# Kernel tuning notes

Measured on AMD Instinct MI355X. Metric: run time of the kernel, lower is better.

## Reference

```python
import jax, jax.numpy as jnp
import numpy as np
import math

T, B = 2048, 32
N_CLASSES = 64
D_MODEL = 512
N_LAYERS = 2
N_HEADS = 8
D_HEAD = 64
D_FF = N_HEADS * D_HEAD * 4  # 2048
E_VAL = (D_MODEL + 1) // 2   # 256 value-embedding dim
D_PE = D_MODEL // 2          # 256 positional dim (concatenated)
EPS_ATTN = 1e-6
EPS_LN = 1e-5


def _pe_table(t, d):
    pos = np.arange(t, dtype=np.float32)[:, None]
    div = np.exp(np.arange(0, d, 2, dtype=np.float32) * (-math.log(10000.0) / d))
    pe = np.zeros((t, d), dtype=np.float32)
    pe[:, 0::2] = np.sin(pos * div)
    pe[:, 1::2] = np.cos(pos * div)
    return jnp.asarray(pe)


def _ln(h, g, b):
    m = jnp.mean(h, axis=-1, keepdims=True)
    v = jnp.mean((h - m) ** 2, axis=-1, keepdims=True)
    return (h - m) * jax.lax.rsqrt(v + EPS_LN) * g + b


def setup_inputs() -> dict:
    key = jax.random.key(0)
    ks = jax.random.split(key, 12)
    s = 0.02
    L, dm, dff = N_LAYERS, D_MODEL, D_FF
    return {
        "x": jax.random.randint(ks[0], (T, B), 0, N_CLASSES),
        "E": jax.random.normal(ks[1], (N_CLASSES, E_VAL)) * s,
        "Wq": jax.random.normal(ks[2], (L, dm, dm)) * s, "bq": jnp.zeros((L, dm)),
        "Wk": jax.random.normal(ks[3], (L, dm, dm)) * s, "bk": jnp.zeros((L, dm)),
        "Wv": jax.random.normal(ks[4], (L, dm, dm)) * s, "bv": jnp.zeros((L, dm)),
        "Wo": jax.random.normal(ks[5], (L, dm, dm)) * s, "bo": jnp.zeros((L, dm)),
        "g1": jnp.ones((L, dm)), "be1": jnp.zeros((L, dm)),
        "W1": jax.random.normal(ks[6], (L, dm, dff)) * s, "b1": jnp.zeros((L, dff)),
        "W2": jax.random.normal(ks[7], (L, dff, dm)) * s, "b2": jnp.zeros((L, dm)),
        "g2": jnp.ones((L, dm)), "be2": jnp.zeros((L, dm)),
        "Wp": jax.random.normal(ks[8], (dm, N_CLASSES)) * s, "bp": jnp.zeros((N_CLASSES,)),
    }


def reference(x, E, Wq, bq, Wk, bk, Wv, bv, Wo, bo, g1, be1, W1, b1, W2, b2, g2, be2, Wp, bp):
    # embed tokens: x [T,B] -> [T,B,E_VAL]; concat positional (broadcast over batch) -> [T,B,D_MODEL]
    emb = E[x]
    pe = _pe_table(T, D_PE)
    h0 = jnp.concatenate([emb, jnp.broadcast_to(pe[:, None, :], (T, B, D_PE))], axis=-1)

    Si0 = jnp.zeros((N_LAYERS, B, N_HEADS, D_HEAD, D_HEAD), h0.dtype)  # sum_t k \otimes v
    Zi0 = jnp.zeros((N_LAYERS, B, N_HEADS, D_HEAD), h0.dtype)          # sum_t k

    phi = lambda u: jax.nn.elu(u) + 1.0  # linear-attention feature map

    def step(carry, xt):
        Si, Zi = carry
        h = xt  # [B, D_MODEL]
        for l in range(N_LAYERS):
            q = phi((h @ Wq[l] + bq[l]).reshape(B, N_HEADS, D_HEAD))
            k = phi((h @ Wk[l] + bk[l]).reshape(B, N_HEADS, D_HEAD))
            v = (h @ Wv[l] + bv[l]).reshape(B, N_HEADS, D_HEAD)
            Sl = Si[l] + k[..., :, None] * v[..., None, :]   # [B,H,D,D]
            Zl = Zi[l] + k
            num = jnp.einsum("bhd,bhdm->bhm", q, Sl)
            den = jnp.einsum("bhd,bhd->bh", q, Zl) + EPS_ATTN
            attn = (num / den[..., None]).reshape(B, N_HEADS * D_HEAD) @ Wo[l] + bo[l]
            h = _ln(h + attn, g1[l], be1[l])
            ff = jax.nn.relu(h @ W1[l] + b1[l]) @ W2[l] + b2[l]
            h = _ln(h + ff, g2[l], be2[l])
            Si = Si.at[l].set(Sl)
            Zi = Zi.at[l].set(Zl)
        return (Si, Zi), h

    _, ys = jax.lax.scan(step, (Si0, Zi0), h0)       # [T,B,D_MODEL]
    y_hat = jnp.transpose(ys, (1, 0, 2)) @ Wp + bp   # [B,T,N_CLASSES]
    return y_hat
```

## Files before the change

### kernel.cpp

```cpp
#include <hip/hip_runtime.h>


typedef unsigned short u16;
typedef __bf16 bf16x8 __attribute__((ext_vector_type(8)));
typedef float f32x4 __attribute__((ext_vector_type(4)));
typedef float f32x16 __attribute__((ext_vector_type(16)));

#define T_SEQ 2048
#define BATCH 32
#define NHEADS 8
#define CT 64
#define NCHUNK 32

#define SKEW(r, k) ((((k) + (((r) >> 3) << 3))) & 63)

__device__ __forceinline__ float b2f(u16 u) {
    union { unsigned int i; float f; } v; v.i = ((unsigned int)u) << 16; return v.f;
}
__device__ __forceinline__ u16 f2b(float f) {
    union { __bf16 b; u16 u; } v; v.b = (__bf16)f; return v.u;
}

__device__ __forceinline__ void gl_lds16(const u16* g, u16* l) {
    __builtin_amdgcn_global_load_lds(
        (const __attribute__((address_space(1))) void*)g,
        (__attribute__((address_space(3))) void*)l,
        16, 0, 0);
}

template<int ACT, bool RES>
__global__ __launch_bounds__(512, 2) void gemm_p8(
    const u16* __restrict__ A, const u16* __restrict__ BT,
    const float* __restrict__ bias, const u16* __restrict__ R,
    u16* __restrict__ C,
    int M, int N, int K, int act_split, int nbn, int GM)
{
    __shared__ __align__(16) u16 AsS[2][256 * 64];
    __shared__ __align__(16) u16 BsS[2][256 * 64];

    const int bid = blockIdx.x;
    const int gsz = GM * nbn;
    const int grp = bid / gsz, rm = bid % gsz;
    const int bm = (grp * GM + rm % GM) * 256;
    const int bn = (rm / GM) * 256;
    if (bm >= M || bn >= N) return;

    const int tid = threadIdx.x;
    const int lane = tid & 63;
    const int w  = tid >> 6;
    const int wr = w >> 2;
    const int wc = w & 3;
    const int l32 = lane & 31;
    const int kh  = lane >> 5;
    const int sr = lane >> 3;
    const int sg = lane & 7;

    const int NT = K >> 6;

    f32x16 acc[4][2] = {};

    auto stage64 = [&](u16* lds, const u16* g, int rowbase, int k0, int row0) {
        const int r = row0 + w * 8 + sr;
        const int gs = sg ^ (r & 7);
        gl_lds16(g + (size_t)(rowbase + r) * K + k0 + gs * 8,
                 lds + (row0 + w * 8) * 64);
    };

    #pragma unroll
    for (int qq = 0; qq < 4; qq++) stage64(AsS[0], A, bm, 0, qq * 64);
    #pragma unroll
    for (int qq = 0; qq < 4; qq++) stage64(BsS[0], BT, bn, 0, qq * 64);
    #pragma unroll
    for (int qq = 0; qq < 4; qq++) stage64(AsS[1], A, bm, 64, qq * 64);
    #pragma unroll
    for (int qq = 0; qq < 4; qq++) stage64(BsS[1], BT, bn, 64, qq * 64);
    asm volatile("s_waitcnt vmcnt(8)" ::: "memory");
    __builtin_amdgcn_s_barrier();

    bf16x8 af[2][4], b0[4], b1[4];

    for (int t = 0; t < NT; ++t) {
        u16* As_ = AsS[t & 1];
        u16* Bs_ = BsS[t & 1];
        const int k2 = (t + 2) << 6;
        const bool pf = (t + 2) < NT;

        #pragma unroll
        for (int mf = 0; mf < 2; mf++) {
            const int r = wr * 128 + mf * 32 + l32;
            #pragma unroll
            for (int ks = 0; ks < 4; ks++) {
                const int gq = (ks * 2 + kh) ^ (r & 7);
                af[mf][ks] = *(const bf16x8*)&As_[r * 64 + gq * 8];
            }
        }
        {
            const int rb = wc * 64 + l32;
            #pragma unroll
            for (int ks = 0; ks < 4; ks++) {
                const int gq = (ks * 2 + kh) ^ (rb & 7);
                b0[ks] = *(const bf16x8*)&Bs_[rb * 64 + gq * 8];
            }
        }
        __builtin_amdgcn_s_barrier();
        asm volatile("s_waitcnt lgkmcnt(0)" ::: "memory");
        __builtin_amdgcn_sched_barrier(0);
        __builtin_amdgcn_s_setprio(1);
        #pragma unroll
        for (int ks = 0; ks < 4; ks++)
            #pragma unroll
            for (int mf = 0; mf < 2; mf++)
                acc[mf][0] = __builtin_amdgcn_mfma_f32_32x32x16_bf16(
                    af[mf][ks], b0[ks], acc[mf][0], 0, 0, 0);
        __builtin_amdgcn_s_setprio(0);
        __builtin_amdgcn_s_barrier();

        {
            const int rb = wc * 64 + 32 + l32;
            #pragma unroll
            for (int ks = 0; ks < 4; ks++) {
                const int gq = (ks * 2 + kh) ^ (rb & 7);
                b1[ks] = *(const bf16x8*)&Bs_[rb * 64 + gq * 8];
            }
        }
        if (pf) { stage64(As_, A, bm, k2, 0); stage64(As_, A, bm, k2, 128); }
        __builtin_amdgcn_s_barrier();
        asm volatile("s_waitcnt lgkmcnt(0)" ::: "memory");
        __builtin_amdgcn_sched_barrier(0);
        __builtin_amdgcn_s_setprio(1);
        #pragma unroll
        for (int ks = 0; ks < 4; ks++)
            #pragma unroll
            for (int mf = 0; mf < 2; mf++)
                acc[mf][1] = __builtin_amdgcn_mfma_f32_32x32x16_bf16(
                    af[mf][ks], b1[ks], acc[mf][1], 0, 0, 0);
        __builtin_amdgcn_s_setprio(0);
        __builtin_amdgcn_s_barrier();

        #pragma unroll
        for (int mf = 0; mf < 2; mf++) {
            const int r = wr * 128 + 64 + mf * 32 + l32;
            #pragma unroll
            for (int ks = 0; ks < 4; ks++) {
                const int gq = (ks * 2 + kh) ^ (r & 7);
                af[mf][ks] = *(const bf16x8*)&As_[r * 64 + gq * 8];
            }
        }
        if (pf) { stage64(Bs_, BT, bn, k2, 0); stage64(Bs_, BT, bn, k2, 64); }
        __builtin_amdgcn_s_barrier();
        asm volatile("s_waitcnt lgkmcnt(0)" ::: "memory");
        __builtin_amdgcn_sched_barrier(0);
        __builtin_amdgcn_s_setprio(1);
        #pragma unroll
        for (int ks = 0; ks < 4; ks++)
            #pragma unroll
            for (int mf = 0; mf < 2; mf++)
                acc[2 + mf][0] = __builtin_amdgcn_mfma_f32_32x32x16_bf16(
                    af[mf][ks], b0[ks], acc[2 + mf][0], 0, 0, 0);
        __builtin_amdgcn_s_setprio(0);
        __builtin_amdgcn_s_barrier();

        if (pf) {
            stage64(Bs_, BT, bn, k2, 128); stage64(Bs_, BT, bn, k2, 192);
            stage64(As_, A,  bm, k2, 64);  stage64(As_, A,  bm, k2, 192);
        }
        __builtin_amdgcn_s_barrier();
        __builtin_amdgcn_s_setprio(1);
        #pragma unroll
        for (int ks = 0; ks < 4; ks++)
            #pragma unroll
            for (int mf = 0; mf < 2; mf++)
                acc[2 + mf][1] = __builtin_amdgcn_mfma_f32_32x32x16_bf16(
                    af[mf][ks], b1[ks], acc[2 + mf][1], 0, 0, 0);
        __builtin_amdgcn_s_setprio(0);
        if (pf) asm volatile("s_waitcnt vmcnt(8)" ::: "memory");
        else    asm volatile("s_waitcnt vmcnt(0)" ::: "memory");
        __builtin_amdgcn_s_barrier();
    }

    #pragma unroll
    for (int i = 0; i < 4; i++) {
        const int row0 = bm + wr * 128 + i * 32 + 4 * kh;
        #pragma unroll
        for (int j = 0; j < 2; j++) {
            const int col = bn + wc * 64 + j * 32 + l32;
            const float bb = bias[col];
            const bool phi = (ACT == 2) && (col < act_split);
            #pragma unroll
            for (int reg = 0; reg < 16; reg++) {
                const int m = row0 + (reg & 3) + 8 * (reg >> 2);
                float v = acc[i][j][reg] + bb;
                if (RES) v += b2f(R[(size_t)m * N + col]);
                if (ACT == 1) v = fmaxf(v, 0.f);
                if (ACT == 2) { if (phi) v = (v > 0.f) ? (v + 1.f) : __expf(v); }
                C[(size_t)m * N + col] = f2b(v);
            }
        }
    }
}

template<int BM, int BN, int WM, int WN>
__global__ __launch_bounds__(WM*WN*64) void gemm_sm(
    const u16* __restrict__ A, const u16* __restrict__ BT,
    const float* __restrict__ bias, float* __restrict__ C,
    int M, int N, int K)
{
    constexpr int BK = 32;
    constexpr int LDT = BK + 8;
    constexpr int NTHR = WM * WN * 64;
    __shared__ __align__(16) u16 As[BM * LDT];
    __shared__ __align__(16) u16 Bs[BN * LDT];

    const int tid = threadIdx.x;
    const int bm = blockIdx.y * BM;
    const int bn = blockIdx.x * BN;
    const int lane = tid & 63;
    const int wid = tid >> 6;
    const int wrow = (wid / WN) * (BM / WM);
    const int wcol = (wid % WN) * (BN / WN);
    constexpr int FM = BM / WM / 16;
    constexpr int FN = BN / WN / 16;
    const int lrow = lane & 15;
    const int lk = (lane >> 4) * 8;

    f32x4 acc[FM][FN] = {};

    for (int k0 = 0; k0 < K; k0 += BK) {
        #pragma unroll
        for (int g0 = 0; g0 < BM * 4; g0 += NTHR) {
            int g = g0 + tid;
            int row = g >> 2, kk = (g & 3) * 8;
            *(uint4*)&As[row * LDT + kk] =
                *(const uint4*)&A[(size_t)(bm + row) * K + k0 + kk];
        }
        #pragma unroll
        for (int g0 = 0; g0 < BN * 4; g0 += NTHR) {
            int g = g0 + tid;
            int row = g >> 2, kk = (g & 3) * 8;
            *(uint4*)&Bs[row * LDT + kk] =
                *(const uint4*)&BT[(size_t)(bn + row) * K + k0 + kk];
        }
        __syncthreads();
        bf16x8 af[FM], bfv[FN];
        #pragma unroll
        for (int i = 0; i < FM; i++)
            af[i] = *(const bf16x8*)&As[(wrow + i * 16 + lrow) * LDT + lk];
        #pragma unroll
        for (int j = 0; j < FN; j++)
            bfv[j] = *(const bf16x8*)&Bs[(wcol + j * 16 + lrow) * LDT + lk];
        #pragma unroll
        for (int i = 0; i < FM; i++)
            #pragma unroll
            for (int j = 0; j < FN; j++)
                acc[i][j] = __builtin_amdgcn_mfma_f32_16x16x32_bf16(
                    bfv[j], af[i], acc[i][j], 0, 0, 0);
        __syncthreads();
    }

    #pragma unroll
    for (int i = 0; i < FM; i++) {
        const int row = bm + wrow + i * 16 + lrow;
        #pragma unroll
        for (int j = 0; j < FN; j++) {
            const int col0 = bn + wcol + j * 16 + (lane >> 4) * 4;
            const float4 bb = *(const float4*)&bias[col0];
            float4 o = { acc[i][j][0] + bb.x, acc[i][j][1] + bb.y,
                         acc[i][j][2] + bb.z, acc[i][j][3] + bb.w };
            *(float4*)&C[(size_t)row * N + col0] = o;
        }
    }
}

__global__ __launch_bounds__(256) void prep_kernel(
    const float* __restrict__ Wq, const float* __restrict__ Wk,
    const float* __restrict__ Wv, const float* __restrict__ Wo,
    const float* __restrict__ W1, const float* __restrict__ W2,
    const float* __restrict__ Wp,
    const float* __restrict__ bq, const float* __restrict__ bk,
    const float* __restrict__ bv,
    u16* __restrict__ qkvT, u16* __restrict__ woT, u16* __restrict__ w1T,
    u16* __restrict__ w2T, u16* __restrict__ wpT, u16* __restrict__ pe,
    float* __restrict__ bqkv)
{
    __shared__ float tile[32][33];
    const int bid = blockIdx.x;
    const float* src; u16* dst; int K, N, bx, by;

    if (bid < 1536) {
        int l = bid / 768, r = bid % 768, m = r >> 8, t = r & 255;
        const float* s3[3] = { Wq, Wk, Wv };
        src = s3[m] + (size_t)l * 262144;
        dst = qkvT + (size_t)l * 786432 + (size_t)m * 262144;
        K = 512; N = 512; bx = t & 15; by = t >> 4;
    } else if (bid < 2048) {
        int r = bid - 1536, l = r >> 8, t = r & 255;
        src = Wo + (size_t)l * 262144; dst = woT + (size_t)l * 262144;
        K = 512; N = 512; bx = t & 15; by = t >> 4;
    } else if (bid < 4096) {
        int r = bid - 2048, l = r >> 10, t = r & 1023;
        src = W1 + (size_t)l * 1048576; dst = w1T + (size_t)l * 1048576;
        K = 512; N = 2048; bx = t & 63; by = t >> 6;
    } else if (bid < 6144) {
        int r = bid - 4096, l = r >> 10, t = r & 1023;
        src = W2 + (size_t)l * 1048576; dst = w2T + (size_t)l * 1048576;
        K = 2048; N = 512; bx = t & 15; by = t >> 4;
    } else if (bid < 6176) {
        int t = bid - 6144;
        src = Wp; dst = wpT; K = 512; N = 64; bx = t & 1; by = t >> 1;
    } else if (bid < 8224) {
        int id = (bid - 6176) * 256 + threadIdx.x;
        int t = id >> 8, j = id & 255;
        int i = j >> 1;
        float div = expf(-(float)(2 * i) * (9.210340371976184f / 256.f));
        float arg = (float)t * div;
        pe[id] = f2b((j & 1) ? cosf(arg) : sinf(arg));
        return;
    } else {
        int id = (bid - 8224) * 256 + threadIdx.x;
        if (id < 3072) {
            int l = id / 1536, i2 = id % 1536;
            float v = (i2 < 512) ? bq[l * 512 + i2]
                    : (i2 < 1024) ? bk[l * 512 + i2 - 512]
                                  : bv[l * 512 + i2 - 1024];
            bqkv[id] = v;
        }
        return;
    }

    int tx = threadIdx.x & 31, ty = threadIdx.x >> 5;
    #pragma unroll
    for (int yy = 0; yy < 4; yy++) {
        int k = by * 32 + ty + yy * 8;
        tile[ty + yy * 8][tx] = src[(size_t)k * N + bx * 32 + tx];
    }
    __syncthreads();
    #pragma unroll
    for (int yy = 0; yy < 4; yy++) {
        int n = bx * 32 + ty + yy * 8;
        dst[(size_t)n * K + by * 32 + tx] = f2b(tile[tx][ty + yy * 8]);
    }
}

__global__ __launch_bounds__(256) void embed_kernel(
    const int* __restrict__ x, const float* __restrict__ E,
    const u16* __restrict__ pe, u16* __restrict__ h, int b0)
{
    int idx = blockIdx.x * 256 + threadIdx.x;
    int e8 = idx * 8;
    int r = e8 >> 9;
    int c = e8 & 511;
    int t = r & (T_SEQ - 1);
    int b = b0 + (r >> 11);
    union { u16 u[8]; uint4 v; } o;
    if (c < 256) {
        const float* Ep = &E[(size_t)x[t * BATCH + b] * 256 + c];
        #pragma unroll
        for (int i = 0; i < 8; i++) o.u[i] = f2b(Ep[i]);
    } else {
        o.v = *(const uint4*)&pe[t * 256 + (c - 256)];
    }
    *(uint4*)&h[e8] = o.v;
}

__global__ __launch_bounds__(256) void attn_chunk_sums(
    const u16* __restrict__ qkv, u16* __restrict__ S, float* __restrict__ Z,
    int BHg)
{
    __shared__ __align__(16) u16 Kt[64 * 72], Vt[64 * 72];
    int bid = blockIdx.x;
    int bh = bid % BHg, c = bid / BHg;
    int bl = bh >> 3, hh = bh & 7;
    {
        const int m  = threadIdx.x & 7;
        const int d0 = m * 8;
        #pragma unroll
        for (int p = 0; p < 2; p++) {
            const int t = p * 32 + (threadIdx.x >> 3);
            size_t rr = ((size_t)(bl * T_SEQ + c * 64 + t)) * 1536 + hh * 64 + d0;
            uint4 kv = *(const uint4*)&qkv[rr + 512];
            uint4 vv = *(const uint4*)&qkv[rr + 1024];
            const u16* kp = (const u16*)&kv;
            const u16* vp = (const u16*)&vv;
            const int sk = (t + d0) & 63;
            u16* kb = &Kt[d0 * 72 + sk];
            u16* vb = &Vt[d0 * 72 + sk];
            #pragma unroll
            for (int s = 0; s < 8; s++) { kb[s * 72] = kp[s]; vb[s * 72] = vp[s]; }
        }
    }
    __syncthreads();
    int lane = threadIdx.x & 63;
    int w = threadIdx.x >> 6;
    int lrow = lane & 15, quad = lane >> 4;
    int m0 = w * 16;
    f32x4 acc[4] = {};
    #pragma unroll
    for (int k0 = 0; k0 < 64; k0 += 32) {
        const int ra = m0 + lrow;
        bf16x8 af = *(const bf16x8*)&Vt[ra * 72 + SKEW(ra, k0 + quad * 8)];
        #pragma unroll
        for (int jt = 0; jt < 4; jt++) {
            const int rb = jt * 16 + lrow;
            bf16x8 bf = *(const bf16x8*)&Kt[rb * 72 + SKEW(rb, k0 + quad * 8)];
            acc[jt] = __builtin_amdgcn_mfma_f32_16x16x32_bf16(bf, af, acc[jt], 0, 0, 0);
        }
    }
    size_t base = ((size_t)c * BHg + bh) * 4096;
    const int m = m0 + lrow;
    #pragma unroll
    for (int jt = 0; jt < 4; jt++) {
        const int d0 = jt * 16 + quad * 4;
        union { u16 q[4]; uint2 u; } pk;
        #pragma unroll
        for (int r = 0; r < 4; r++) pk.q[r] = f2b(acc[jt][r]);
        *(uint2*)&S[base + m * 64 + d0] = pk.u;
    }
    if (threadIdx.x < 64) {
        const int d = threadIdx.x;
        float z = 0.f;
        #pragma unroll
        for (int t8 = 0; t8 < 64; t8 += 8) {
            bf16x8 kk = *(const bf16x8*)&Kt[d * 72 + SKEW(d, t8)];
            #pragma unroll
            for (int u = 0; u < 8; u++) z += (float)kk[u];
        }
        Z[((size_t)c * BHg + bh) * 64 + d] = z;
    }
}

__global__ __launch_bounds__(256) void attn_prefix(
    u16* __restrict__ S, float* __restrict__ Z, int BHg)
{
    int gid = blockIdx.x * 256 + threadIdx.x;
    int bh = gid >> 12, e = gid & 4095;
    size_t stride = (size_t)BHg * 4096;
    size_t base = (size_t)bh * 4096 + e;
    float v[NCHUNK];
    #pragma unroll
    for (int c = 0; c < NCHUNK; c++) v[c] = b2f(S[base + c * stride]);
    float run = 0.f;
    #pragma unroll
    for (int c = 0; c < NCHUNK; c++) {
        float t = v[c]; S[base + c * stride] = f2b(run); run += t;
    }
    if (gid < BHg * 64) {
        size_t zb = (size_t)gid;
        size_t zs = (size_t)BHg * 64;
        float zv[NCHUNK];
        #pragma unroll
        for (int c = 0; c < NCHUNK; c++) zv[c] = Z[zb + c * zs];
        float zr = 0.f;
        #pragma unroll
        for (int c = 0; c < NCHUNK; c++) {
            float t = zv[c]; Z[zb + c * zs] = zr; zr += t;
        }
    }
}

__global__ __launch_bounds__(256) void attn_intra(
    const u16* __restrict__ qkv, const u16* __restrict__ Sp,
    const float* __restrict__ Zp, u16* __restrict__ out, int BHg)
{
    __shared__ __align__(16) u16 Qs[64 * 72], Ks[64 * 72], Vt[64 * 72],
                                 Ssh[64 * 72];
    __shared__ float Zsh[64], den2sh[64], den1sh[64];
    u16* Ps = Ks;
    int bid = blockIdx.x;
    int bh = bid % BHg, c = bid / BHg;
    int bl = bh >> 3, hh = bh & 7;
    size_t sbase = ((size_t)c * BHg + bh) * 4096;
    {
        const int m  = threadIdx.x & 7;
        const int d0 = m * 8;
        #pragma unroll
        for (int p = 0; p < 2; p++) {
            const int t = p * 32 + (threadIdx.x >> 3);
            size_t rr = ((size_t)(bl * T_SEQ + c * 64 + t)) * 1536 + hh * 64 + d0;
            *(uint4*)&Qs[t * 72 + d0]  = *(const uint4*)&qkv[rr];
            *(uint4*)&Ks[t * 72 + d0]  = *(const uint4*)&qkv[rr + 512];
            *(uint4*)&Ssh[t * 72 + d0] = *(const uint4*)&Sp[sbase + t * 64 + d0];
            uint4 vv = *(const uint4*)&qkv[rr + 1024];
            const u16* vp = (const u16*)&vv;
            const int sk = (t + d0) & 63;
            u16* vb = &Vt[d0 * 72 + sk];
            #pragma unroll
            for (int s = 0; s < 8; s++) vb[s * 72] = vp[s];
        }
    }
    if (threadIdx.x < 64)
        Zsh[threadIdx.x] = Zp[((size_t)c * BHg + bh) * 64 + threadIdx.x];
    __syncthreads();

    if (threadIdx.x < 64) {
        float s = 0.f;
        #pragma unroll
        for (int d8 = 0; d8 < 64; d8 += 8) {
            bf16x8 qq = *(const bf16x8*)&Qs[threadIdx.x * 72 + d8];
            #pragma unroll
            for (int u = 0; u < 8; u++) s += (float)qq[u] * Zsh[d8 + u];
        }
        den2sh[threadIdx.x] = s;
    }

    int lane = threadIdx.x & 63;
    int w = threadIdx.x >> 6;
    int lrow = lane & 15, quad = lane >> 4;
    int i0 = w * 16;

    f32x4 accp[4] = {};
    #pragma unroll
    for (int k0 = 0; k0 < 64; k0 += 32) {
        bf16x8 af = *(const bf16x8*)&Qs[(i0 + lrow) * 72 + k0 + quad * 8];
        #pragma unroll
        for (int jt = 0; jt < 4; jt++) {
            bf16x8 bf = *(const bf16x8*)&Ks[(jt * 16 + lrow) * 72 + k0 + quad * 8];
            accp[jt] = __builtin_amdgcn_mfma_f32_16x16x32_bf16(af, bf, accp[jt], 0, 0, 0);
        }
    }
    __syncthreads();
    #pragma unroll
    for (int r = 0; r < 4; r++) {
        int row = i0 + quad * 4 + r;
        float d1 = 0.f;
        #pragma unroll
        for (int jt = 0; jt < 4; jt++) {
            int col = jt * 16 + lrow;
            float pv = (col <= row) ? accp[jt][r] : 0.f;
            d1 += pv;
            Ps[row * 72 + col] = f2b(pv);
        }
        #pragma unroll
        for (int off = 1; off < 16; off <<= 1)
            d1 += __shfl_xor(d1, off, 64);
        if (lrow == 0) den1sh[row] = d1;
    }
    __syncthreads();

    f32x4 acco[4] = {};
    #pragma unroll
    for (int k0 = 0; k0 < 64; k0 += 32) {
        bf16x8 ps = *(const bf16x8*)&Ps[(i0 + lrow) * 72 + k0 + quad * 8];
        #pragma unroll
        for (int jt = 0; jt < 4; jt++) {
            const int rv = jt * 16 + lrow;
            bf16x8 vf = *(const bf16x8*)&Vt[rv * 72 + SKEW(rv, k0 + quad * 8)];
            acco[jt] = __builtin_amdgcn_mfma_f32_16x16x32_bf16(vf, ps, acco[jt], 0, 0, 0);
        }
    }
    #pragma unroll
    for (int k0 = 0; k0 < 64; k0 += 32) {
        bf16x8 qf = *(const bf16x8*)&Qs[(i0 + lrow) * 72 + k0 + quad * 8];
        #pragma unroll
        for (int jt = 0; jt < 4; jt++) {
            bf16x8 sf = *(const bf16x8*)&Ssh[(jt * 16 + lrow) * 72 + k0 + quad * 8];
            acco[jt] = __builtin_amdgcn_mfma_f32_16x16x32_bf16(sf, qf, acco[jt], 0, 0, 0);
        }
    }
    const int i = i0 + lrow;
    const float inv = 1.f / (den1sh[i] + den2sh[i] + 1e-6f);
    size_t orow = ((size_t)(bl * T_SEQ + c * 64 + i)) * 512 + hh * 64;
    #pragma unroll
    for (int jt = 0; jt < 4; jt++) {
        const int m0 = jt * 16 + quad * 4;
        union { u16 q[4]; uint2 u; } pk;
        #pragma unroll
        for (int r = 0; r < 4; r++) pk.q[r] = f2b(acco[jt][r] * inv);
        *(uint2*)&out[orow + m0] = pk.u;
    }
}

__global__ __launch_bounds__(256) void ln_kernel(
    const u16* __restrict__ s_in,
    const float* __restrict__ g, const float* __restrict__ be, u16* __restrict__ out)
{
    int row = blockIdx.x * 4 + (threadIdx.x >> 6);
    int lane = threadIdx.x & 63;
    size_t base = (size_t)row * 512 + lane * 8;
    uint4 hv = *(const uint4*)&s_in[base];
    const u16* hp = (const u16*)&hv;
    float x[8]; float s = 0.f;
    #pragma unroll
    for (int i = 0; i < 8; i++) { x[i] = b2f(hp[i]); s += x[i]; }
    #pragma unroll
    for (int off = 32; off > 0; off >>= 1) s += __shfl_xor(s, off, 64);
    float m = s * (1.f / 512.f);
    float vs = 0.f;
    #pragma unroll
    for (int i = 0; i < 8; i++) { float t = x[i] - m; vs += t * t; }
    #pragma unroll
    for (int off = 32; off > 0; off >>= 1) vs += __shfl_xor(vs, off, 64);
    float rstd = rsqrtf(vs * (1.f / 512.f) + 1e-5f);
    union { u16 u[8]; uint4 v; } o;
    #pragma unroll
    for (int i = 0; i < 8; i++)
        o.u[i] = f2b((x[i] - m) * rstd * g[lane * 8 + i] + be[lane * 8 + i]);
    *(uint4*)&out[base] = o.v;
}

extern "C" void kernel_launch(void* const* d_in, const int* in_sizes, int n_in,
                              void* d_out, int out_size, void* d_ws, size_t ws_size,
                              hipStream_t stream)
{
    const int*   x  = (const int*)d_in[0];
    const float* E  = (const float*)d_in[1];
    const float* Wq = (const float*)d_in[2];
    const float* bq = (const float*)d_in[3];
    const float* Wk = (const float*)d_in[4];
    const float* bk = (const float*)d_in[5];
    const float* Wv = (const float*)d_in[6];
    const float* bv = (const float*)d_in[7];
    const float* Wo = (const float*)d_in[8];
    const float* bo = (const float*)d_in[9];
    const float* g1 = (const float*)d_in[10];
    const float* be1= (const float*)d_in[11];
    const float* W1 = (const float*)d_in[12];
    const float* b1 = (const float*)d_in[13];
    const float* W2 = (const float*)d_in[14];
    const float* b2 = (const float*)d_in[15];
    const float* g2 = (const float*)d_in[16];
    const float* be2= (const float*)d_in[17];
    const float* Wp = (const float*)d_in[18];
    const float* bp = (const float*)d_in[19];

    char* p = (char*)d_ws;
    u16* qkvT = (u16*)p; p += (size_t)2 * 1536 * 512 * 2;
    u16* woT  = (u16*)p; p += (size_t)2 * 512 * 512 * 2;
    u16* w1T  = (u16*)p; p += (size_t)2 * 2048 * 512 * 2;
    u16* w2T  = (u16*)p; p += (size_t)2 * 512 * 2048 * 2;
    u16* wpT  = (u16*)p; p += (size_t)64 * 512 * 2;
    u16* pe   = (u16*)p; p += (size_t)T_SEQ * 256 * 2;
    float* bqkv = (float*)p; p += (size_t)16384;
    size_t fixed = (size_t)(p - (char*)d_ws);

    const size_t perB = 12648448ULL;
    int Bg = 32;
    while (Bg > 1 && fixed + (size_t)Bg * perB > ws_size) Bg >>= 1;
    const int rows = Bg * T_SEQ;
    const int BHg = Bg * NHEADS;
    const int nbm = rows / 256;

    u16* h      = (u16*)p; p += (size_t)rows * 512 * 2;
    u16* qkvBig = (u16*)p; p += (size_t)rows * 2048 * 2;
    u16* am     = (u16*)p; p += (size_t)rows * 512 * 2;
    float* Z    = (float*)p; p += (size_t)BHg * NCHUNK * 64 * 4;
    u16* qkv = qkvBig;
    u16* Sb  = qkvBig + (size_t)rows * 1536;
    u16* ff1 = qkvBig;
    u16* o_  = qkvBig;

    dim3 blk(256);
    dim3 blk8(512);

    prep_kernel<<<8236, blk, 0, stream>>>(
        Wq, Wk, Wv, Wo, W1, W2, Wp, bq, bk, bv,
        qkvT, woT, w1T, w2T, wpT, pe, bqkv);

    for (int b0 = 0; b0 < BATCH; b0 += Bg) {
        embed_kernel<<<rows / 4, blk, 0, stream>>>(x, E, pe, h, b0);

        for (int l = 0; l < 2; l++) {
            gemm_p8<2, false><<<dim3(nbm * 6), blk8, 0, stream>>>(
                h, qkvT + (size_t)l * 786432, bqkv + l * 1536, nullptr, qkv,
                rows, 1536, 512, 1024, 6, 8);
            attn_chunk_sums<<<NCHUNK * BHg, blk, 0, stream>>>(qkv, Sb, Z, BHg);
            attn_prefix<<<BHg * 16, blk, 0, stream>>>(Sb, Z, BHg);
            attn_intra<<<NCHUNK * BHg, blk, 0, stream>>>(qkv, Sb, Z, am, BHg);
            gemm_p8<0, true><<<dim3(nbm * 2), blk8, 0, stream>>>(
                am, woT + (size_t)l * 262144, bo + l * 512, h, o_,
                rows, 512, 512, 0, 2, 8);
            ln_kernel<<<rows / 4, blk, 0, stream>>>(o_, g1 + l * 512, be1 + l * 512, h);
            gemm_p8<1, false><<<dim3(nbm * 8), blk8, 0, stream>>>(
                h, w1T + (size_t)l * 1048576, b1 + l * 2048, nullptr, ff1,
                rows, 2048, 512, 0, 8, 8);
            gemm_p8<0, true><<<dim3(nbm * 2), blk8, 0, stream>>>(
                ff1, w2T + (size_t)l * 1048576, b2 + l * 512, h, am,
                rows, 512, 2048, 0, 2, 8);
            ln_kernel<<<rows / 4, blk, 0, stream>>>(am, g2 + l * 512, be2 + l * 512, h);
        }

        gemm_sm<64, 64, 2, 2><<<dim3(1, rows / 64), blk, 0, stream>>>(
            h, wpT, bp, (float*)d_out + (size_t)b0 * T_SEQ * 64, rows, 64, 512);
    }

    (void)in_sizes; (void)n_in; (void)out_size; (void)ws_size;
}
```

Before: 1.535 ms.

## Restructure GEMM main loop from four to two MFMA phases per K-tile

Reorganizes the bf16 GEMM's per-tile schedule from four barrier-separated MFMA phases into two. Both B fragments are loaded up front, and the A half-tile for row groups 64/192 of the next tile is staged one iteration ahead, so the other loads can be grouped. This cuts barrier and waitcnt overhead per K-step and gives longer uninterrupted MFMA bursts. In exchange it raises register pressure, since b0 and b1 are live together, and it depends on the altered vmcnt accounting and prefetch ordering being correct.

```diff
diff --git a/kernel.cpp b/kernel.cpp
--- a/kernel.cpp
+++ b/kernel.cpp
@@ -70,11 +70,11 @@
     for (int qq = 0; qq < 4; qq++) stage64(AsS[0], A, bm, 0, qq * 64);
     #pragma unroll
     for (int qq = 0; qq < 4; qq++) stage64(BsS[0], BT, bn, 0, qq * 64);
-    #pragma unroll
-    for (int qq = 0; qq < 4; qq++) stage64(AsS[1], A, bm, 64, qq * 64);
+    stage64(AsS[1], A, bm, 64, 0);
+    stage64(AsS[1], A, bm, 64, 128);
     #pragma unroll
     for (int qq = 0; qq < 4; qq++) stage64(BsS[1], BT, bn, 64, qq * 64);
-    asm volatile("s_waitcnt vmcnt(8)" ::: "memory");
+    asm volatile("s_waitcnt vmcnt(6)" ::: "memory");
     __builtin_amdgcn_s_barrier();
 
     bf16x8 af[2][4], b0[4], b1[4];
@@ -82,8 +82,11 @@
     for (int t = 0; t < NT; ++t) {
         u16* As_ = AsS[t & 1];
         u16* Bs_ = BsS[t & 1];
+        u16* An1 = AsS[(t + 1) & 1];
+        const int k1 = (t + 1) << 6;
         const int k2 = (t + 2) << 6;
-        const bool pf = (t + 2) < NT;
+        const bool pf1 = (t + 1) < NT;
+        const bool pf2 = (t + 2) < NT;
 
         #pragma unroll
         for (int mf = 0; mf < 2; mf++) {
@@ -101,7 +104,14 @@
                 const int gq = (ks * 2 + kh) ^ (rb & 7);
                 b0[ks] = *(const bf16x8*)&Bs_[rb * 64 + gq * 8];
             }
-        }
+            const int rb1 = wc * 64 + 32 + l32;
+            #pragma unroll
+            for (int ks = 0; ks < 4; ks++) {
+                const int gq = (ks * 2 + kh) ^ (rb1 & 7);
+                b1[ks] = *(const bf16x8*)&Bs_[rb1 * 64 + gq * 8];
+            }
+        }
+        if (pf1) { stage64(An1, A, bm, k1, 64); stage64(An1, A, bm, k1, 192); }
         __builtin_amdgcn_s_barrier();
         asm volatile("s_waitcnt lgkmcnt(0)" ::: "memory");
         __builtin_amdgcn_sched_barrier(0);
@@ -109,21 +119,29 @@
         #pragma unroll
         for (int ks = 0; ks < 4; ks++)
             #pragma unroll
-            for (int mf = 0; mf < 2; mf++)
+            for (int mf = 0; mf < 2; mf++) {
                 acc[mf][0] = __builtin_amdgcn_mfma_f32_32x32x16_bf16(
                     af[mf][ks], b0[ks], acc[mf][0], 0, 0, 0);
+                acc[mf][1] = __builtin_amdgcn_mfma_f32_32x32x16_bf16(
+                    af[mf][ks], b1[ks], acc[mf][1], 0, 0, 0);
+            }
         __builtin_amdgcn_s_setprio(0);
         __builtin_amdgcn_s_barrier();
 
-        {
-            const int rb = wc * 64 + 32 + l32;
+        #pragma unroll
+        for (int mf = 0; mf < 2; mf++) {
+            const int r = wr * 128 + 64 + mf * 32 + l32;
             #pragma unroll
             for (int ks = 0; ks < 4; ks++) {
-                const int gq = (ks * 2 + kh) ^ (rb & 7);
-                b1[ks] = *(const bf16x8*)&Bs_[rb * 64 + gq * 8];
+                const int gq = (ks * 2 + kh) ^ (r & 7);
+                af[mf][ks] = *(const bf16x8*)&As_[r * 64 + gq * 8];
             }
         }
-        if (pf) { stage64(As_, A, bm, k2, 0); stage64(As_, A, bm, k2, 128); }
+        if (pf2) {
+            stage64(As_, A,  bm, k2, 0);   stage64(As_, A,  bm, k2, 128);
+            stage64(Bs_, BT, bn, k2, 0);   stage64(Bs_, BT, bn, k2, 64);
+            stage64(Bs_, BT, bn, k2, 128); stage64(Bs_, BT, bn, k2, 192);
+        }
         __builtin_amdgcn_s_barrier();
         asm volatile("s_waitcnt lgkmcnt(0)" ::: "memory");
         __builtin_amdgcn_sched_barrier(0);
@@ -131,50 +149,15 @@
         #pragma unroll
         for (int ks = 0; ks < 4; ks++)
             #pragma unroll
-            for (int mf = 0; mf < 2; mf++)
-                acc[mf][1] = __builtin_amdgcn_mfma_f32_32x32x16_bf16(
-                    af[mf][ks], b1[ks], acc[mf][1], 0, 0, 0);
-        __builtin_amdgcn_s_setprio(0);
-        __builtin_amdgcn_s_barrier();
-
-        #pragma unroll
-        for (int mf = 0; mf < 2; mf++) {
-            const int r = wr * 128 + 64 + mf * 32 + l32;
-            #pragma unroll
-            for (int ks = 0; ks < 4; ks++) {
-                const int gq = (ks * 2 + kh) ^ (r & 7);
-                af[mf][ks] = *(const bf16x8*)&As_[r * 64 + gq * 8];
-            }
-        }
-        if (pf) { stage64(Bs_, BT, bn, k2, 0); stage64(Bs_, BT, bn, k2, 64); }
-        __builtin_amdgcn_s_barrier();
-        asm volatile("s_waitcnt lgkmcnt(0)" ::: "memory");
-        __builtin_amdgcn_sched_barrier(0);
-        __builtin_amdgcn_s_setprio(1);
-        #pragma unroll
-        for (int ks = 0; ks < 4; ks++)
-            #pragma unroll
-            for (int mf = 0; mf < 2; mf++)
+            for (int mf = 0; mf < 2; mf++) {
                 acc[2 + mf][0] = __builtin_amdgcn_mfma_f32_32x32x16_bf16(
                     af[mf][ks], b0[ks], acc[2 + mf][0], 0, 0, 0);
-        __builtin_amdgcn_s_setprio(0);
-        __builtin_amdgcn_s_barrier();
-
-        if (pf) {
-            stage64(Bs_, BT, bn, k2, 128); stage64(Bs_, BT, bn, k2, 192);
-            stage64(As_, A,  bm, k2, 64);  stage64(As_, A,  bm, k2, 192);
-        }
-        __builtin_amdgcn_s_barrier();
-        __builtin_amdgcn_s_setprio(1);
-        #pragma unroll
-        for (int ks = 0; ks < 4; ks++)
-            #pragma unroll
-            for (int mf = 0; mf < 2; mf++)
                 acc[2 + mf][1] = __builtin_amdgcn_mfma_f32_32x32x16_bf16(
                     af[mf][ks], b1[ks], acc[2 + mf][1], 0, 0, 0);
+            }
         __builtin_amdgcn_s_setprio(0);
-        if (pf) asm volatile("s_waitcnt vmcnt(8)" ::: "memory");
-        else    asm volatile("s_waitcnt vmcnt(0)" ::: "memory");
+        if (pf2) asm volatile("s_waitcnt vmcnt(6)" ::: "memory");
+        else     asm volatile("s_waitcnt vmcnt(0)" ::: "memory");
         __builtin_amdgcn_s_barrier();
     }
 
```

Result: no change. 1.525 ms (-0.7%).
